# Performance work log

Hardware: AMD Instinct MI355X
Metric: run time of the kernel (lower is better)

## Reference

```python
import jax, jax.numpy as jnp
import numpy as np

N_NODES, N_EDGES, DIM, N_LAYERS, N_GRAPHS, N_CLASSES = 50000, 640000, 128, 5, 512, 128


def setup_inputs() -> dict:
    key = jax.random.key(0)
    ks = jax.random.split(key, 10)
    x = jnp.zeros((N_NODES,), dtype=jnp.int32)  # Embedding(1, D) -> all indices 0
    edge_index = jax.random.randint(ks[0], (2, N_EDGES), 0, N_NODES, dtype=jnp.int32)
    edge_attr = jax.random.normal(ks[1], (N_EDGES, DIM), dtype=jnp.float32)
    batch = jnp.sort(jax.random.randint(ks[2], (N_NODES,), 0, N_GRAPHS, dtype=jnp.int32))
    s = 1.0 / np.sqrt(DIM)
    node_emb = jax.random.normal(ks[3], (1, DIM), dtype=jnp.float32)
    Ws = jax.random.normal(ks[4], (N_LAYERS, DIM, DIM), dtype=jnp.float32) * s
    bs = jnp.zeros((N_LAYERS, DIM), dtype=jnp.float32)
    Wes = jax.random.normal(ks[5], (N_LAYERS, DIM, DIM), dtype=jnp.float32) * s
    Wp = jax.random.normal(ks[6], (DIM, N_CLASSES), dtype=jnp.float32) * s
    bp = jnp.zeros((N_CLASSES,), dtype=jnp.float32)
    return {"x": x, "edge_index": edge_index, "edge_attr": edge_attr, "batch": batch,
            "node_emb": node_emb, "Ws": Ws, "bs": bs, "Wes": Wes, "Wp": Wp, "bp": bp}


def reference(x, edge_index, edge_attr, batch, node_emb, Ws, bs, Wes, Wp, bp):
    src, dst = edge_index[0], edge_index[1]
    h = node_emb[x]  # [N, D] embedding lookup (vocab=1)
    n = h.shape[0]
    e = src.shape[0]
    deg = jax.ops.segment_sum(jnp.ones((e,), h.dtype), dst, num_segments=n)
    deg = jnp.maximum(deg, 1.0)[:, None]  # mean aggregation denominator
    for l in range(N_LAYERS):
        hw = h @ Ws[l] + bs[l]                       # [N, D]
        msg = hw[src] + edge_attr @ Wes[l]           # [E, D] gather + edge transform
        agg = jax.ops.segment_sum(msg, dst, num_segments=n) / deg  # scatter-mean
        h = agg + hw                                 # root connection
        if l < N_LAYERS - 1:
            h = jax.nn.relu(h)                       # relu on all but last layer
        # dropout is identity in eval mode
    g = N_GRAPHS
    cnt = jnp.maximum(jax.ops.segment_sum(jnp.ones((n,), h.dtype), batch, num_segments=g), 1.0)
    pooled = jax.ops.segment_sum(h, batch, num_segments=g) / cnt[:, None]  # global_mean_pool
    return pooled @ Wp + bp  # [G, num_clases]
```

## Files before the change

### kernel.cpp

```cpp
#include <hip/hip_runtime.h>

#define N_NODES   50000
#define N_EDGES   640000
#define DIM       128
#define N_LAYERS  5
#define N_GRAPHS  512
#define N_CLASSES 128
#define NB_SCAN   196

typedef __attribute__((ext_vector_type(8))) short short8;
typedef __attribute__((ext_vector_type(4))) float floatx4;

__device__ inline float bfhi(unsigned u) { return __uint_as_float(u & 0xffff0000u); }
__device__ inline float bflo(unsigned u) { return __uint_as_float(u << 16); }
__device__ inline unsigned f2bf(float f) {
  unsigned x = __float_as_uint(f);
  return (x + 0x7fffu + ((x >> 16) & 1u)) >> 16;
}

__global__ void k_zero(int* __restrict__ deg, int* __restrict__ fill,
                       float* __restrict__ pool, float* __restrict__ cnt) {
  int i = blockIdx.x * 256 + threadIdx.x;
  if (i < N_NODES) { deg[i] = 0; fill[i] = 0; }
  if (i < N_GRAPHS * DIM) pool[i] = 0.f;
  if (i < N_GRAPHS) cnt[i] = 0.f;
}

__global__ void k_deg(const int* __restrict__ dst, int* __restrict__ deg) {
  int e = blockIdx.x * 256 + threadIdx.x;
  if (e < N_EDGES) atomicAdd(&deg[dst[e]], 1);
}

__global__ void k_scan1(const int* __restrict__ deg, int* __restrict__ bsum) {
  __shared__ int s[256];
  int t = threadIdx.x, i = blockIdx.x * 256 + t;
  s[t] = (i < N_NODES) ? deg[i] : 0;
  __syncthreads();
  for (int o = 128; o > 0; o >>= 1) {
    if (t < o) s[t] += s[t + o];
    __syncthreads();
  }
  if (t == 0) bsum[blockIdx.x] = s[0];
}

__global__ void k_scan2(int* __restrict__ bsum) {
  __shared__ int s[256];
  int t = threadIdx.x;
  s[t] = (t < NB_SCAN) ? bsum[t] : 0;
  __syncthreads();
  for (int o = 1; o < 256; o <<= 1) {
    int add = (t >= o) ? s[t - o] : 0;
    __syncthreads();
    s[t] += add;
    __syncthreads();
  }
  int ex = (t == 0) ? 0 : s[t - 1];
  if (t < NB_SCAN) bsum[t] = ex;
}

__global__ void k_scan3(const int* __restrict__ deg, const int* __restrict__ bsum,
                        int* __restrict__ row_ptr) {
  __shared__ int s[256];
  int t = threadIdx.x, i = blockIdx.x * 256 + t;
  s[t] = (i < N_NODES) ? deg[i] : 0;
  __syncthreads();
  for (int o = 1; o < 256; o <<= 1) {
    int add = (t >= o) ? s[t - o] : 0;
    __syncthreads();
    s[t] += add;
    __syncthreads();
  }
  int ex = bsum[blockIdx.x] + ((t == 0) ? 0 : s[t - 1]);
  if (i < N_NODES) row_ptr[i] = ex;
  if (blockIdx.x == 0 && t == 0) row_ptr[N_NODES] = N_EDGES;
}

__global__ void k_fill(const int* __restrict__ src, const int* __restrict__ dst,
                       const int* __restrict__ row_ptr, int* __restrict__ fill,
                       int2* __restrict__ col) {
  int e = blockIdx.x * 256 + threadIdx.x;
  if (e < N_EDGES) {
    int d = dst[e];
    int pos = row_ptr[d] + atomicAdd(&fill[d], 1);
    col[pos] = make_int2(src[e], e);
  }
}

__global__ void k_wconv(const float* __restrict__ Ws, const float* __restrict__ Wes,
                        unsigned short* __restrict__ Wt_s, unsigned short* __restrict__ Wt_e) {
  int idx = blockIdx.x * 256 + threadIdx.x;
  int which = idx / (N_LAYERS * DIM * DIM);
  int rem = idx - which * (N_LAYERS * DIM * DIM);
  int l = rem >> 14;
  int c = (rem >> 7) & 127;
  int k = rem & 127;
  const float* W = which ? Wes : Ws;
  unsigned short* O = which ? Wt_e : Wt_s;
  float v = W[((size_t)l * DIM + k) * DIM + c];
  O[((size_t)l * DIM + c) * DIM + k] = (unsigned short)f2bf(v);
}

__global__ void k_v0(const float* __restrict__ node_emb, const float* __restrict__ Ws0,
                     float* __restrict__ v0) {
  int c = threadIdx.x;
  float acc = 0.f;
  for (int k = 0; k < DIM; k++) acc += node_emb[k] * Ws0[(size_t)k * DIM + c];
  v0[c] = acc;
}

__global__ void k_ean_init(const int* __restrict__ row_ptr, const int2* __restrict__ col,
                           const float* __restrict__ edge_attr,
                           unsigned short* __restrict__ ean, float* __restrict__ rdeg) {
  int sub = threadIdx.x >> 5;
  int lane = threadIdx.x & 31;
  int i = blockIdx.x * 8 + sub;
  if (i >= N_NODES) return;
  int b = row_ptr[i], e = row_ptr[i + 1];
  float ax = 0.f, ay = 0.f, az = 0.f, aw = 0.f;
  int p = b;
  for (; p + 2 <= e; p += 2) {
    int e0 = col[p].y, e1 = col[p + 1].y;
    float4 v0 = ((const float4*)(edge_attr + (size_t)e0 * DIM))[lane];
    float4 v1 = ((const float4*)(edge_attr + (size_t)e1 * DIM))[lane];
    ax += v0.x + v1.x; ay += v0.y + v1.y; az += v0.z + v1.z; aw += v0.w + v1.w;
  }
  if (p < e) {
    int e0 = col[p].y;
    float4 v0 = ((const float4*)(edge_attr + (size_t)e0 * DIM))[lane];
    ax += v0.x; ay += v0.y; az += v0.z; aw += v0.w;
  }
  float r = 1.0f / (float)max(e - b, 1);
  if (lane == 0) rdeg[i] = r;
  uint2 o;
  o.x = f2bf(ax * r) | (f2bf(ay * r) << 16);
  o.y = f2bf(az * r) | (f2bf(aw * r) << 16);
  ((uint2*)(ean + (size_t)i * DIM))[lane] = o;
}

__global__ __launch_bounds__(256) void k_gemm0(
    const unsigned short* __restrict__ ean, const unsigned short* __restrict__ W1,
    const float* __restrict__ v0, const float* __restrict__ bias,
    const int* __restrict__ deg, unsigned short* __restrict__ hout) {
  __shared__ unsigned short sA[64][72];
  __shared__ unsigned short sW[128][72];
  int tid = threadIdx.x;
  int wave = tid >> 6, lane = tid & 63;
  int quad = lane >> 4, l16 = lane & 15;
  int row0 = blockIdx.x * 64;
  floatx4 acc[8];
  #pragma unroll
  for (int ci = 0; ci < 8; ci++) acc[ci] = (floatx4){0.f, 0.f, 0.f, 0.f};

  for (int kc = 0; kc < 128; kc += 64) {
    __syncthreads();
    #pragma unroll
    for (int q = 0; q < 2; q++) {
      int s = tid + 256 * q;
      int r = s >> 3, seg = s & 7;
      int grow = row0 + r;
      uint4 v = make_uint4(0u, 0u, 0u, 0u);
      if (grow < N_NODES)
        v = *(const uint4*)(ean + (size_t)grow * DIM + kc + seg * 8);
      *(uint4*)(&sA[r][seg * 8]) = v;
    }
    #pragma unroll
    for (int q = 0; q < 4; q++) {
      int s = tid + 256 * q;
      int r = s >> 3, seg = s & 7;
      *(uint4*)(&sW[r][seg * 8]) =
          *(const uint4*)(W1 + (size_t)r * DIM + kc + seg * 8);
    }
    __syncthreads();
    #pragma unroll
    for (int ks = 0; ks < 64; ks += 32) {
      short8 a = *(const short8*)(&sA[wave * 16 + l16][ks + quad * 8]);
      #pragma unroll
      for (int ci = 0; ci < 8; ci++) {
        short8 b = *(const short8*)(&sW[ci * 16 + l16][ks + quad * 8]);
        acc[ci] = __builtin_amdgcn_mfma_f32_16x16x32_bf16(a, b, acc[ci], 0, 0, 0);
      }
    }
  }
  #pragma unroll
  for (int ci = 0; ci < 8; ci++) {
    int col = ci * 16 + l16;
    float bv = bias[col];
    float vv = v0[col];
    #pragma unroll
    for (int r = 0; r < 4; r++) {
      int row = row0 + wave * 16 + quad * 4 + r;
      if (row < N_NODES) {
        float s = (deg[row] > 0) ? 2.f : 1.f;
        float v = acc[ci][r] + bv + s * vv;
        v = fmaxf(v, 0.f);
        hout[(size_t)row * DIM + col] = (unsigned short)f2bf(v);
      }
    }
  }
}

#define ACC8(v) { a0 += bflo(v.x); a1 += bfhi(v.x); a2 += bflo(v.y); a3 += bfhi(v.y); \
                  a4 += bflo(v.z); a5 += bfhi(v.z); a6 += bflo(v.w); a7 += bfhi(v.w); }

__global__ __launch_bounds__(256) void k_layer(
    const int* __restrict__ row_ptr, const int2* __restrict__ col,
    const unsigned short* __restrict__ hin, const float* __restrict__ rdeg,
    const unsigned short* __restrict__ ean,
    const unsigned short* __restrict__ W0, const unsigned short* __restrict__ W1,
    const float* __restrict__ bias, unsigned short* __restrict__ hout, int relu) {
  __shared__ unsigned short sU[64][136];
  __shared__ unsigned short sE[64][136];
  __shared__ unsigned short sW[128][72];
  int tid = threadIdx.x;
  int row0 = blockIdx.x * 64;

  #pragma unroll
  for (int q = 0; q < 4; q++) {
    int s = tid + 256 * q;
    int r = s >> 4, seg = s & 15;
    int grow = row0 + r;
    uint4 v = make_uint4(0u, 0u, 0u, 0u);
    if (grow < N_NODES) v = *(const uint4*)(ean + (size_t)grow * DIM + seg * 8);
    *(uint4*)(&sE[r][seg * 8]) = v;
  }

  {
    int g = tid >> 4, lane = tid & 15;
    for (int n = 0; n < 4; n++) {
      int r = g + n * 16;
      int i = row0 + r;
      if (i < N_NODES) {
        int b = row_ptr[i], e = row_ptr[i + 1];
        float a0 = 0.f, a1 = 0.f, a2 = 0.f, a3 = 0.f,
              a4 = 0.f, a5 = 0.f, a6 = 0.f, a7 = 0.f;
        int p = b;
        for (; p + 4 <= e; p += 4) {
          int j0 = col[p].x, j1 = col[p + 1].x, j2 = col[p + 2].x, j3 = col[p + 3].x;
          uint4 v0 = *(const uint4*)(hin + (size_t)j0 * DIM + lane * 8);
          uint4 v1 = *(const uint4*)(hin + (size_t)j1 * DIM + lane * 8);
          uint4 v2 = *(const uint4*)(hin + (size_t)j2 * DIM + lane * 8);
          uint4 v3 = *(const uint4*)(hin + (size_t)j3 * DIM + lane * 8);
          ACC8(v0); ACC8(v1); ACC8(v2); ACC8(v3);
        }
        for (; p < e; p++) {
          int j0 = col[p].x;
          uint4 v0 = *(const uint4*)(hin + (size_t)j0 * DIM + lane * 8);
          ACC8(v0);
        }
        float rr = rdeg[i];
        uint4 hv = *(const uint4*)(hin + (size_t)i * DIM + lane * 8);
        uint4 o;
        o.x = f2bf(bflo(hv.x) + a0 * rr) | (f2bf(bfhi(hv.x) + a1 * rr) << 16);
        o.y = f2bf(bflo(hv.y) + a2 * rr) | (f2bf(bfhi(hv.y) + a3 * rr) << 16);
        o.z = f2bf(bflo(hv.z) + a4 * rr) | (f2bf(bfhi(hv.z) + a5 * rr) << 16);
        o.w = f2bf(bflo(hv.w) + a6 * rr) | (f2bf(bfhi(hv.w) + a7 * rr) << 16);
        *(uint4*)(&sU[r][lane * 8]) = o;
      } else {
        *(uint4*)(&sU[r][lane * 8]) = make_uint4(0u, 0u, 0u, 0u);
      }
    }
  }

  int wave = tid >> 6, lane = tid & 63;
  int quad = lane >> 4, l16 = lane & 15;
  floatx4 acc[8];
  #pragma unroll
  for (int ci = 0; ci < 8; ci++) acc[ci] = (floatx4){0.f, 0.f, 0.f, 0.f};

  for (int m = 0; m < 2; m++) {
    const unsigned short* W = m ? W1 : W0;
    for (int kc = 0; kc < 128; kc += 64) {
      __syncthreads();
      #pragma unroll
      for (int q = 0; q < 4; q++) {
        int s = tid + 256 * q;
        int r = s >> 3, seg = s & 7;
        *(uint4*)(&sW[r][seg * 8]) =
            *(const uint4*)(W + (size_t)r * DIM + kc + seg * 8);
      }
      __syncthreads();
      #pragma unroll
      for (int ks = 0; ks < 64; ks += 32) {
        short8 a = m ? *(const short8*)(&sE[wave * 16 + l16][kc + ks + quad * 8])
                     : *(const short8*)(&sU[wave * 16 + l16][kc + ks + quad * 8]);
        #pragma unroll
        for (int ci = 0; ci < 8; ci++) {
          short8 b = *(const short8*)(&sW[ci * 16 + l16][ks + quad * 8]);
          acc[ci] = __builtin_amdgcn_mfma_f32_16x16x32_bf16(a, b, acc[ci], 0, 0, 0);
        }
      }
    }
  }
  #pragma unroll
  for (int ci = 0; ci < 8; ci++) {
    int col_ = ci * 16 + l16;
    float bv = bias[col_];
    #pragma unroll
    for (int r = 0; r < 4; r++) {
      int row = row0 + wave * 16 + quad * 4 + r;
      if (row < N_NODES) {
        float v = acc[ci][r] + bv;
        if (relu) v = fmaxf(v, 0.f);
        hout[(size_t)row * DIM + col_] = (unsigned short)f2bf(v);
      }
    }
  }
}

__global__ void k_pool(const unsigned short* __restrict__ h, const int* __restrict__ batch,
                       float* __restrict__ pool, float* __restrict__ cnt) {
  int t = threadIdx.x;
  int i0 = blockIdx.x * 128;
  int iend = min(i0 + 128, N_NODES);
  float acc = 0.f;
  int cur = -1, run = 0;
  for (int i = i0; i < iend; i++) {
    int g = batch[i];
    if (g != cur) {
      if (cur >= 0) {
        atomicAdd(&pool[(size_t)cur * DIM + t], acc);
        if (t == 0) atomicAdd(&cnt[cur], (float)run);
      }
      acc = 0.f; run = 0; cur = g;
    }
    acc += __uint_as_float(((unsigned)h[(size_t)i * DIM + t]) << 16);
    run++;
  }
  if (cur >= 0) {
    atomicAdd(&pool[(size_t)cur * DIM + t], acc);
    if (t == 0) atomicAdd(&cnt[cur], (float)run);
  }
}

__global__ void k_out(const float* __restrict__ pool, const float* __restrict__ cnt,
                      const float* __restrict__ Wp, const float* __restrict__ bp,
                      float* __restrict__ out) {
  __shared__ float sp[DIM];
  int g = blockIdx.x, t = threadIdx.x;
  sp[t] = pool[(size_t)g * DIM + t];
  __syncthreads();
  float r = 1.0f / fmaxf(cnt[g], 1.0f);
  float acc = 0.f;
  for (int k = 0; k < DIM; k++) acc += sp[k] * Wp[(size_t)k * N_CLASSES + t];
  out[(size_t)g * N_CLASSES + t] = acc * r + bp[t];
}

extern "C" void kernel_launch(void* const* d_in, const int* in_sizes, int n_in,
                              void* d_out, int out_size, void* d_ws, size_t ws_size,
                              hipStream_t stream) {
  (void)in_sizes; (void)n_in; (void)out_size; (void)ws_size;
  const int*   x          = (const int*)d_in[0];
  const int*   edge_index = (const int*)d_in[1];
  const float* edge_attr  = (const float*)d_in[2];
  const int*   batch      = (const int*)d_in[3];
  const float* node_emb   = (const float*)d_in[4];
  const float* Ws         = (const float*)d_in[5];
  const float* bs         = (const float*)d_in[6];
  const float* Wes        = (const float*)d_in[7];
  const float* Wp         = (const float*)d_in[8];
  const float* bp         = (const float*)d_in[9];
  (void)x;
  float* out = (float*)d_out;
  const int* src = edge_index;
  const int* dst = edge_index + N_EDGES;

  char* p = (char*)d_ws;
  auto alloc = [&](size_t bytes) {
    void* q = (void*)p;
    p += (bytes + 255) & ~(size_t)255;
    return q;
  };
  unsigned short* h    = (unsigned short*)alloc((size_t)N_NODES * DIM * 2);
  unsigned short* h2   = (unsigned short*)alloc((size_t)N_NODES * DIM * 2);
  unsigned short* ean  = (unsigned short*)alloc((size_t)N_NODES * DIM * 2);
  unsigned short* Wt_s = (unsigned short*)alloc((size_t)N_LAYERS * DIM * DIM * 2);
  unsigned short* Wt_e = (unsigned short*)alloc((size_t)N_LAYERS * DIM * DIM * 2);
  int*   deg     = (int*)  alloc((size_t)N_NODES * 4);
  float* rdeg    = (float*)alloc((size_t)N_NODES * 4);
  int*   row_ptr = (int*)  alloc((size_t)(N_NODES + 64) * 4);
  int*   fill    = (int*)  alloc((size_t)N_NODES * 4);
  int2*  col     = (int2*) alloc((size_t)N_EDGES * 8);
  float* pool    = (float*)alloc((size_t)N_GRAPHS * DIM * 4);
  float* cnt     = (float*)alloc((size_t)N_GRAPHS * 4);
  int*   bsum    = (int*)  alloc(256 * 4);
  float* v0      = (float*)alloc(DIM * 4);

  k_zero<<<256, 256, 0, stream>>>(deg, fill, pool, cnt);
  k_deg<<<(N_EDGES + 255) / 256, 256, 0, stream>>>(dst, deg);
  k_scan1<<<NB_SCAN, 256, 0, stream>>>(deg, bsum);
  k_scan2<<<1, 256, 0, stream>>>(bsum);
  k_scan3<<<NB_SCAN, 256, 0, stream>>>(deg, bsum, row_ptr);
  k_fill<<<(N_EDGES + 255) / 256, 256, 0, stream>>>(src, dst, row_ptr, fill, col);
  k_wconv<<<(2 * N_LAYERS * DIM * DIM) / 256, 256, 0, stream>>>(Ws, Wes, Wt_s, Wt_e);
  k_v0<<<1, DIM, 0, stream>>>(node_emb, Ws, v0);
  k_ean_init<<<(N_NODES + 7) / 8, 256, 0, stream>>>(row_ptr, col, edge_attr, ean, rdeg);

  k_gemm0<<<(N_NODES + 63) / 64, 256, 0, stream>>>(
      ean, Wt_e, v0, bs, deg, h);
  const unsigned short* hin = h;
  unsigned short* hout = h2;
  for (int l = 1; l < N_LAYERS; l++) {
    k_layer<<<(N_NODES + 63) / 64, 256, 0, stream>>>(
        row_ptr, col, hin, rdeg, ean,
        Wt_s + (size_t)l * DIM * DIM, Wt_e + (size_t)l * DIM * DIM,
        bs + (size_t)l * DIM, hout, (l < N_LAYERS - 1) ? 1 : 0);
    const unsigned short* tmp = hout; hout = (unsigned short*)hin; hin = tmp;
  }
  k_pool<<<(N_NODES + 127) / 128, 128, 0, stream>>>(h, batch, pool, cnt);
  k_out<<<N_GRAPHS, N_CLASSES, 0, stream>>>(pool, cnt, Wp, bp, out);
}
```

Baseline: 848.5 us.

## Fuse all GNN layers into one persistent cooperative kernel with grid sync

Replaces the separate first-layer GEMM kernel and the four per-layer launches with a single cooperative kernel. Its blocks loop over 64-row tiles and call a grid-wide sync between layers, with the first-layer special cases handled by branches on the layer index. The grid is sized from occupancy queries to keep every block resident. The aim is to remove inter-kernel launch gaps and tail effects, at the cost of grid-barrier overhead and possible load imbalance, since tiles are strided across a fixed grid.

```diff
diff --git a/kernel.cpp b/kernel.cpp
--- a/kernel.cpp
+++ b/kernel.cpp
@@ -1,4 +1,7 @@
 #include <hip/hip_runtime.h>
+#include <hip/hip_cooperative_groups.h>
+
+namespace cg = cooperative_groups;
 
 #define N_NODES   50000
 #define N_EDGES   640000
@@ -7,6 +10,7 @@
 #define N_GRAPHS  512
 #define N_CLASSES 128
 #define NB_SCAN   196
+#define NT        ((N_NODES + 63) / 64)
 
 typedef __attribute__((ext_vector_type(8))) short short8;
 typedef __attribute__((ext_vector_type(4))) float floatx4;
@@ -137,173 +141,136 @@
   ((uint2*)(ean + (size_t)i * DIM))[lane] = o;
 }
 
-__global__ __launch_bounds__(256) void k_gemm0(
-    const unsigned short* __restrict__ ean, const unsigned short* __restrict__ W1,
-    const float* __restrict__ v0, const float* __restrict__ bias,
-    const int* __restrict__ deg, unsigned short* __restrict__ hout) {
-  __shared__ unsigned short sA[64][72];
+#define ACC8(v) { a0 += bflo(v.x); a1 += bfhi(v.x); a2 += bflo(v.y); a3 += bfhi(v.y); \
+                  a4 += bflo(v.z); a5 += bfhi(v.z); a6 += bflo(v.w); a7 += bfhi(v.w); }
+
+__global__ __launch_bounds__(256) void k_layers(
+    const int* __restrict__ row_ptr, const int2* __restrict__ col,
+    const float* __restrict__ rdeg, const unsigned short* __restrict__ ean,
+    const unsigned short* __restrict__ Wt_s, const unsigned short* __restrict__ Wt_e,
+    const float* __restrict__ bs, const float* __restrict__ v0,
+    const int* __restrict__ deg, unsigned short* __restrict__ hA,
+    unsigned short* __restrict__ hB) {
+  cg::grid_group gg = cg::this_grid();
+  __shared__ unsigned short sU[64][136];
+  __shared__ unsigned short sE[64][136];
   __shared__ unsigned short sW[128][72];
   int tid = threadIdx.x;
   int wave = tid >> 6, lane = tid & 63;
   int quad = lane >> 4, l16 = lane & 15;
-  int row0 = blockIdx.x * 64;
-  floatx4 acc[8];
-  #pragma unroll
-  for (int ci = 0; ci < 8; ci++) acc[ci] = (floatx4){0.f, 0.f, 0.f, 0.f};
-
-  for (int kc = 0; kc < 128; kc += 64) {
-    __syncthreads();
-    #pragma unroll
-    for (int q = 0; q < 2; q++) {
-      int s = tid + 256 * q;
-      int r = s >> 3, seg = s & 7;
-      int grow = row0 + r;
-      uint4 v = make_uint4(0u, 0u, 0u, 0u);
-      if (grow < N_NODES)
-        v = *(const uint4*)(ean + (size_t)grow * DIM + kc + seg * 8);
-      *(uint4*)(&sA[r][seg * 8]) = v;
-    }
-    #pragma unroll
-    for (int q = 0; q < 4; q++) {
-      int s = tid + 256 * q;
-      int r = s >> 3, seg = s & 7;
-      *(uint4*)(&sW[r][seg * 8]) =
-          *(const uint4*)(W1 + (size_t)r * DIM + kc + seg * 8);
-    }
-    __syncthreads();
-    #pragma unroll
-    for (int ks = 0; ks < 64; ks += 32) {
-      short8 a = *(const short8*)(&sA[wave * 16 + l16][ks + quad * 8]);
-      #pragma unroll
-      for (int ci = 0; ci < 8; ci++) {
-        short8 b = *(const short8*)(&sW[ci * 16 + l16][ks + quad * 8]);
-        acc[ci] = __builtin_amdgcn_mfma_f32_16x16x32_bf16(a, b, acc[ci], 0, 0, 0);
-      }
-    }
-  }
-  #pragma unroll
-  for (int ci = 0; ci < 8; ci++) {
-    int col = ci * 16 + l16;
-    float bv = bias[col];
-    float vv = v0[col];
-    #pragma unroll
-    for (int r = 0; r < 4; r++) {
-      int row = row0 + wave * 16 + quad * 4 + r;
-      if (row < N_NODES) {
-        float s = (deg[row] > 0) ? 2.f : 1.f;
-        float v = acc[ci][r] + bv + s * vv;
-        v = fmaxf(v, 0.f);
-        hout[(size_t)row * DIM + col] = (unsigned short)f2bf(v);
-      }
-    }
-  }
-}
-
-#define ACC8(v) { a0 += bflo(v.x); a1 += bfhi(v.x); a2 += bflo(v.y); a3 += bfhi(v.y); \
-                  a4 += bflo(v.z); a5 += bfhi(v.z); a6 += bflo(v.w); a7 += bfhi(v.w); }
-
-__global__ __launch_bounds__(256) void k_layer(
-    const int* __restrict__ row_ptr, const int2* __restrict__ col,
-    const unsigned short* __restrict__ hin, const float* __restrict__ rdeg,
-    const unsigned short* __restrict__ ean,
-    const unsigned short* __restrict__ W0, const unsigned short* __restrict__ W1,
-    const float* __restrict__ bias, unsigned short* __restrict__ hout, int relu) {
-  __shared__ unsigned short sU[64][136];
-  __shared__ unsigned short sE[64][136];
-  __shared__ unsigned short sW[128][72];
-  int tid = threadIdx.x;
-  int row0 = blockIdx.x * 64;
-
-  #pragma unroll
-  for (int q = 0; q < 4; q++) {
-    int s = tid + 256 * q;
-    int r = s >> 4, seg = s & 15;
-    int grow = row0 + r;
-    uint4 v = make_uint4(0u, 0u, 0u, 0u);
-    if (grow < N_NODES) v = *(const uint4*)(ean + (size_t)grow * DIM + seg * 8);
-    *(uint4*)(&sE[r][seg * 8]) = v;
-  }
-
-  {
-    int g = tid >> 4, lane = tid & 15;
-    for (int n = 0; n < 4; n++) {
-      int r = g + n * 16;
-      int i = row0 + r;
-      if (i < N_NODES) {
-        int b = row_ptr[i], e = row_ptr[i + 1];
-        float a0 = 0.f, a1 = 0.f, a2 = 0.f, a3 = 0.f,
-              a4 = 0.f, a5 = 0.f, a6 = 0.f, a7 = 0.f;
-        int p = b;
-        for (; p + 4 <= e; p += 4) {
-          int j0 = col[p].x, j1 = col[p + 1].x, j2 = col[p + 2].x, j3 = col[p + 3].x;
-          uint4 v0 = *(const uint4*)(hin + (size_t)j0 * DIM + lane * 8);
-          uint4 v1 = *(const uint4*)(hin + (size_t)j1 * DIM + lane * 8);
-          uint4 v2 = *(const uint4*)(hin + (size_t)j2 * DIM + lane * 8);
-          uint4 v3 = *(const uint4*)(hin + (size_t)j3 * DIM + lane * 8);
-          ACC8(v0); ACC8(v1); ACC8(v2); ACC8(v3);
-        }
-        for (; p < e; p++) {
-          int j0 = col[p].x;
-          uint4 v0 = *(const uint4*)(hin + (size_t)j0 * DIM + lane * 8);
-          ACC8(v0);
-        }
-        float rr = rdeg[i];
-        uint4 hv = *(const uint4*)(hin + (size_t)i * DIM + lane * 8);
-        uint4 o;
-        o.x = f2bf(bflo(hv.x) + a0 * rr) | (f2bf(bfhi(hv.x) + a1 * rr) << 16);
-        o.y = f2bf(bflo(hv.y) + a2 * rr) | (f2bf(bfhi(hv.y) + a3 * rr) << 16);
-        o.z = f2bf(bflo(hv.z) + a4 * rr) | (f2bf(bfhi(hv.z) + a5 * rr) << 16);
-        o.w = f2bf(bflo(hv.w) + a6 * rr) | (f2bf(bfhi(hv.w) + a7 * rr) << 16);
-        *(uint4*)(&sU[r][lane * 8]) = o;
-      } else {
-        *(uint4*)(&sU[r][lane * 8]) = make_uint4(0u, 0u, 0u, 0u);
-      }
-    }
-  }
-
-  int wave = tid >> 6, lane = tid & 63;
-  int quad = lane >> 4, l16 = lane & 15;
-  floatx4 acc[8];
-  #pragma unroll
-  for (int ci = 0; ci < 8; ci++) acc[ci] = (floatx4){0.f, 0.f, 0.f, 0.f};
-
-  for (int m = 0; m < 2; m++) {
-    const unsigned short* W = m ? W1 : W0;
-    for (int kc = 0; kc < 128; kc += 64) {
+
+  const unsigned short* hin = hA;
+  unsigned short* hout = hA;
+
+  for (int l = 0; l < N_LAYERS; l++) {
+    const unsigned short* W0 = Wt_s + (size_t)l * DIM * DIM;
+    const unsigned short* W1 = Wt_e + (size_t)l * DIM * DIM;
+    const float* bias = bs + (size_t)l * DIM;
+    int relu = (l < N_LAYERS - 1);
+
+    for (int tile = blockIdx.x; tile < NT; tile += gridDim.x) {
+      int row0 = tile * 64;
       __syncthreads();
+
       #pragma unroll
       for (int q = 0; q < 4; q++) {
         int s = tid + 256 * q;
-        int r = s >> 3, seg = s & 7;
-        *(uint4*)(&sW[r][seg * 8]) =
-            *(const uint4*)(W + (size_t)r * DIM + kc + seg * 8);
-      }
-      __syncthreads();
+        int r = s >> 4, seg = s & 15;
+        int grow = row0 + r;
+        uint4 v = make_uint4(0u, 0u, 0u, 0u);
+        if (grow < N_NODES) v = *(const uint4*)(ean + (size_t)grow * DIM + seg * 8);
+        *(uint4*)(&sE[r][seg * 8]) = v;
+      }
+
+      if (l > 0) {
+        int g = tid >> 4, glane = tid & 15;
+        for (int n = 0; n < 4; n++) {
+          int r = g + n * 16;
+          int i = row0 + r;
+          if (i < N_NODES) {
+            int b = row_ptr[i], e = row_ptr[i + 1];
+            float a0 = 0.f, a1 = 0.f, a2 = 0.f, a3 = 0.f,
+                  a4 = 0.f, a5 = 0.f, a6 = 0.f, a7 = 0.f;
+            int p = b;
+            for (; p + 4 <= e; p += 4) {
+              int j0 = col[p].x, j1 = col[p + 1].x, j2 = col[p + 2].x, j3 = col[p + 3].x;
+              uint4 w0 = *(const uint4*)(hin + (size_t)j0 * DIM + glane * 8);
+              uint4 w1 = *(const uint4*)(hin + (size_t)j1 * DIM + glane * 8);
+              uint4 w2 = *(const uint4*)(hin + (size_t)j2 * DIM + glane * 8);
+              uint4 w3 = *(const uint4*)(hin + (size_t)j3 * DIM + glane * 8);
+              ACC8(w0); ACC8(w1); ACC8(w2); ACC8(w3);
+            }
+            for (; p < e; p++) {
+              int j0 = col[p].x;
+              uint4 w0 = *(const uint4*)(hin + (size_t)j0 * DIM + glane * 8);
+              ACC8(w0);
+            }
+            float rr = rdeg[i];
+            uint4 hv = *(const uint4*)(hin + (size_t)i * DIM + glane * 8);
+            uint4 o;
+            o.x = f2bf(bflo(hv.x) + a0 * rr) | (f2bf(bfhi(hv.x) + a1 * rr) << 16);
+            o.y = f2bf(bflo(hv.y) + a2 * rr) | (f2bf(bfhi(hv.y) + a3 * rr) << 16);
+            o.z = f2bf(bflo(hv.z) + a4 * rr) | (f2bf(bfhi(hv.z) + a5 * rr) << 16);
+            o.w = f2bf(bflo(hv.w) + a6 * rr) | (f2bf(bfhi(hv.w) + a7 * rr) << 16);
+            *(uint4*)(&sU[r][glane * 8]) = o;
+          } else {
+            *(uint4*)(&sU[r][glane * 8]) = make_uint4(0u, 0u, 0u, 0u);
+          }
+        }
+      }
+
+      floatx4 acc[8];
       #pragma unroll
-      for (int ks = 0; ks < 64; ks += 32) {
-        short8 a = m ? *(const short8*)(&sE[wave * 16 + l16][kc + ks + quad * 8])
-                     : *(const short8*)(&sU[wave * 16 + l16][kc + ks + quad * 8]);
+      for (int ci = 0; ci < 8; ci++) acc[ci] = (floatx4){0.f, 0.f, 0.f, 0.f};
+
+      int mstart = (l == 0) ? 1 : 0;
+      for (int m = mstart; m < 2; m++) {
+        const unsigned short* W = m ? W1 : W0;
+        const unsigned short (*sA)[136] = m ? sE : sU;
+        for (int kc = 0; kc < 128; kc += 64) {
+          __syncthreads();
+          #pragma unroll
+          for (int q = 0; q < 4; q++) {
+            int s = tid + 256 * q;
+            int r = s >> 3, seg = s & 7;
+            *(uint4*)(&sW[r][seg * 8]) =
+                *(const uint4*)(W + (size_t)r * DIM + kc + seg * 8);
+          }
+          __syncthreads();
+          #pragma unroll
+          for (int ks = 0; ks < 64; ks += 32) {
+            short8 a = *(const short8*)(&sA[wave * 16 + l16][kc + ks + quad * 8]);
+            #pragma unroll
+            for (int ci = 0; ci < 8; ci++) {
+              short8 b = *(const short8*)(&sW[ci * 16 + l16][ks + quad * 8]);
+              acc[ci] = __builtin_amdgcn_mfma_f32_16x16x32_bf16(a, b, acc[ci], 0, 0, 0);
+            }
+          }
+        }
+      }
+
+      #pragma unroll
+      for (int ci = 0; ci < 8; ci++) {
+        int col_ = ci * 16 + l16;
+        float bv = bias[col_];
+        float vv = (l == 0) ? v0[col_] : 0.f;
         #pragma unroll
-        for (int ci = 0; ci < 8; ci++) {
-          short8 b = *(const short8*)(&sW[ci * 16 + l16][ks + quad * 8]);
-          acc[ci] = __builtin_amdgcn_mfma_f32_16x16x32_bf16(a, b, acc[ci], 0, 0, 0);
+        for (int r = 0; r < 4; r++) {
+          int row = row0 + wave * 16 + quad * 4 + r;
+          if (row < N_NODES) {
+            float v = acc[ci][r] + bv;
+            if (l == 0) v += ((deg[row] > 0) ? 2.f : 1.f) * vv;
+            if (relu) v = fmaxf(v, 0.f);
+            hout[(size_t)row * DIM + col_] = (unsigned short)f2bf(v);
+          }
         }
       }
     }
-  }
-  #pragma unroll
-  for (int ci = 0; ci < 8; ci++) {
-    int col_ = ci * 16 + l16;
-    float bv = bias[col_];
-    #pragma unroll
-    for (int r = 0; r < 4; r++) {
-      int row = row0 + wave * 16 + quad * 4 + r;
-      if (row < N_NODES) {
-        float v = acc[ci][r] + bv;
-        if (relu) v = fmaxf(v, 0.f);
-        hout[(size_t)row * DIM + col_] = (unsigned short)f2bf(v);
-      }
-    }
+
+    if (l < N_LAYERS - 1) gg.sync();
+
+    if (l == 0) { hin = hA; hout = hB; }
+    else { const unsigned short* t = hin; hin = hout; hout = (unsigned short*)t; }
   }
 }
 
@@ -355,7 +322,7 @@
   const int*   batch      = (const int*)d_in[3];
   const float* node_emb   = (const float*)d_in[4];
   const float* Ws         = (const float*)d_in[5];
-  const float* bs         = (const float*)d_in[6];
+  const float* bsin       = (const float*)d_in[6];
   const float* Wes        = (const float*)d_in[7];
   const float* Wp         = (const float*)d_in[8];
   const float* bp         = (const float*)d_in[9];
@@ -395,17 +362,29 @@
   k_v0<<<1, DIM, 0, stream>>>(node_emb, Ws, v0);
   k_ean_init<<<(N_NODES + 7) / 8, 256, 0, stream>>>(row_ptr, col, edge_attr, ean, rdeg);
 
-  k_gemm0<<<(N_NODES + 63) / 64, 256, 0, stream>>>(
-      ean, Wt_e, v0, bs, deg, h);
-  const unsigned short* hin = h;
-  unsigned short* hout = h2;
-  for (int l = 1; l < N_LAYERS; l++) {
-    k_layer<<<(N_NODES + 63) / 64, 256, 0, stream>>>(
-        row_ptr, col, hin, rdeg, ean,
-        Wt_s + (size_t)l * DIM * DIM, Wt_e + (size_t)l * DIM * DIM,
-        bs + (size_t)l * DIM, hout, (l < N_LAYERS - 1) ? 1 : 0);
-    const unsigned short* tmp = hout; hout = (unsigned short*)hin; hin = tmp;
-  }
+  {
+    int maxb = 0;
+    hipError_t oe = hipOccupancyMaxActiveBlocksPerMultiprocessor(&maxb, k_layers, 256, 0);
+    if (oe != hipSuccess || maxb < 1) maxb = 1;
+    int grid = maxb * 256;
+    if (grid > NT) grid = NT;
+    const int*            a_row_ptr = row_ptr;
+    const int2*           a_col     = col;
+    const float*          a_rdeg    = rdeg;
+    const unsigned short* a_ean     = ean;
+    const unsigned short* a_Wt_s    = Wt_s;
+    const unsigned short* a_Wt_e    = Wt_e;
+    const float*          a_bs      = bsin;
+    const float*          a_v0      = v0;
+    const int*            a_deg     = deg;
+    unsigned short*       a_hA      = h;
+    unsigned short*       a_hB      = h2;
+    void* args[] = {&a_row_ptr, &a_col, &a_rdeg, &a_ean, &a_Wt_s, &a_Wt_e,
+                    &a_bs, &a_v0, &a_deg, &a_hA, &a_hB};
+    hipLaunchCooperativeKernel((void*)k_layers, dim3(grid), dim3(256),
+                               args, 0, stream);
+  }
+
   k_pool<<<(N_NODES + 127) / 128, 128, 0, stream>>>(h, batch, pool, cnt);
   k_out<<<N_GRAPHS, N_CLASSES, 0, stream>>>(pool, cnt, Wp, bp, out);
 }
```

Result: slower. 1.213 ms (+43.0%).
